# Kernel optimization log

Hardware: AMD Instinct MI355X
Metric: run time of the kernel (lower is better)

Reference implementation:

```python
import jax, jax.numpy as jnp
import numpy as np

N, T, D, P, Q = 256, 4096, 64, 4, 4
COEF_SCALE = 0.15  # keeps ARMA stationary over long T


def setup_inputs() -> dict:
    key = jax.random.key(0)
    k_eps, k_phi, k_theta, k_mu = jax.random.split(key, 4)
    eps = jax.random.normal(k_eps, (N, T, D), dtype=jnp.float32)
    phi = COEF_SCALE * jax.random.normal(k_phi, (D, P), dtype=jnp.float32)
    theta = COEF_SCALE * jax.random.normal(k_theta, (D, Q), dtype=jnp.float32)
    mu = jax.random.normal(k_mu, (D,), dtype=jnp.float32)
    x0 = jnp.zeros((N, D), dtype=jnp.float32)
    return {"eps": eps, "phi": phi, "theta": theta, "mu": mu, "x0": x0}


def reference(eps, phi, theta, mu, x0):
    # eps: (N,T,d); phi: (d,p); theta: (d,q); mu: (d,); x0: (N,d)
    n, t, d = eps.shape
    p = phi.shape[1]
    q = theta.shape[1]
    # x history: most-recent-first, [x0, 0, ..., 0] (matches torch padding of x_hist)
    xh0 = jnp.concatenate([x0[:, :, None], jnp.zeros((n, d, p - 1), eps.dtype)], axis=-1)
    eh0 = jnp.zeros((n, d, q), eps.dtype)  # eps history starts as zeros

    def step(carry, e_t):
        xh, eh = carry  # (n,d,p), (n,d,q)
        ar = jnp.einsum('ndp,dp->nd', xh, phi)
        ma = jnp.einsum('ndq,dq->nd', eh, theta)
        x_t = mu[None, :] + ar + e_t + ma  # (n,d)
        xh = jnp.concatenate([x_t[:, :, None], xh[:, :, :-1]], axis=-1)
        eh = jnp.concatenate([e_t[:, :, None], eh[:, :, :-1]], axis=-1)
        return (xh, eh), x_t

    _, xs = jax.lax.scan(step, (xh0, eh0), jnp.swapaxes(eps, 0, 1))  # xs: (T,N,d)
    return jnp.swapaxes(xs, 0, 1)  # (N,T,d)
```

## Files before the change

kernel.cpp:

```cpp
#include <hip/hip_runtime.h>
#include <stdint.h>


typedef float f32x4 __attribute__((ext_vector_type(4)));

constexpr int N = 256;
constexpr int T = 4096;
constexpr int D = 64;
constexpr int P = 4;
constexpr int Q = 4;

constexpr int K = 8;
constexpr int L = 512;
constexpr int B = 256;
constexpr int U = 16;
constexpr int NB = 4;
constexpr int NDMA = (U * D * sizeof(float)) / 1024;

__global__ __launch_bounds__(64, 2)
void arma_wide_kernel(const float* __restrict__ eps,
                      const float* __restrict__ phi,
                      const float* __restrict__ theta,
                      const float* __restrict__ mu,
                      const float* __restrict__ x0,
                      float* __restrict__ out) {
    const int lane = threadIdx.x;
    const int k = blockIdx.x % K;
    const int n = blockIdx.x / K;

    const float ph0 = phi[lane * P + 0];
    const float ph1 = phi[lane * P + 1];
    const float ph2 = phi[lane * P + 2];
    const float ph3 = phi[lane * P + 3];
    const float th0 = theta[lane * Q + 0];
    const float th1 = theta[lane * Q + 1];
    const float th2 = theta[lane * Q + 2];
    const float th3 = theta[lane * Q + 3];
    const float m   = mu[lane];

    const int t0   = k * L;
    const int ts   = (k == 0) ? 0 : t0 - B;
    const int tend = t0 + L;
    const int nit  = (tend - ts) / U;
    const int SB   = (t0 - ts) / U;

    const float* gbase = eps + (size_t)n * T * D;
    float*       obase = out + (size_t)n * T * D;

    const int lt  = lane >> 4;
    const int ld4 = (lane & 15) * 4;

    __shared__ float lbuf[NB][U * D];
    __shared__ float sbuf[U * D];

    float x1, x2, x3, x4, e1, e2, e3, e4;
    x1 = x2 = x3 = x4 = 0.f;
    e1 = e2 = e3 = e4 = 0.f;
    if (k == 0) {
        x1 = x0[n * D + lane];
    } else {
        e1 = gbase[(size_t)(ts - 1) * D + lane];
        e2 = gbase[(size_t)(ts - 2) * D + lane];
        e3 = gbase[(size_t)(ts - 3) * D + lane];
        e4 = gbase[(size_t)(ts - 4) * D + lane];
    }

    auto issue = [&](int b, int t) {
#pragma unroll
        for (int i = 0; i < NDMA; ++i) {
            const float* src = gbase + (size_t)(t + i * 4 + lt) * D + ld4;
            __builtin_amdgcn_global_load_lds(
                (const __attribute__((address_space(1))) void*)src,
                (__attribute__((address_space(3))) void*)&lbuf[b][i * 256],
                16, 0, 0);
        }
    };

    auto compute = [&](int b) {
#pragma unroll
        for (int u = 0; u < U; ++u) {
            const float e = lbuf[b][u * D + lane];
            float acc = m + e;
            acc = fmaf(th0, e1, acc);
            acc = fmaf(th1, e2, acc);
            acc = fmaf(th2, e3, acc);
            acc = fmaf(th3, e4, acc);
            acc = fmaf(ph3, x4, acc);
            acc = fmaf(ph2, x3, acc);
            acc = fmaf(ph1, x2, acc);
            const float x = fmaf(ph0, x1, acc);
            x4 = x3; x3 = x2; x2 = x1; x1 = x;
            e4 = e3; e3 = e2; e2 = e1; e1 = e;
            sbuf[u * D + lane] = x;
        }
    };

    auto flush = [&](int t) {
#pragma unroll
        for (int i = 0; i < 4; ++i) {
            const int row = i * 4 + lt;
            const f32x4 v = *reinterpret_cast<const f32x4*>(&sbuf[row * D + ld4]);
            __builtin_nontemporal_store(
                v, reinterpret_cast<f32x4*>(&obase[(size_t)(t + row) * D + ld4]));
        }
    };

    issue(0, ts);
    issue(1, ts + U);
    issue(2, ts + 2 * U);

    for (int j = 0; j < nit; ++j) {
        const int t = ts + j * U;
        int tpre = t + 3 * U;
        if (tpre > tend - U) tpre = tend - U;
        issue((j + 3) & (NB - 1), tpre);

        const int d = j - SB;
        if (d <= 0) {
            asm volatile("s_waitcnt vmcnt(12)" ::: "memory");
        } else if (d == 1) {
            asm volatile("s_waitcnt vmcnt(16)" ::: "memory");
        } else if (d == 2) {
            asm volatile("s_waitcnt vmcnt(20)" ::: "memory");
        } else {
            asm volatile("s_waitcnt vmcnt(24)" ::: "memory");
        }
        __builtin_amdgcn_sched_barrier(0);

        compute(j & (NB - 1));
        if (j >= SB) flush(t);
    }
}

extern "C" void kernel_launch(void* const* d_in, const int* in_sizes, int n_in,
                              void* d_out, int out_size, void* d_ws, size_t ws_size,
                              hipStream_t stream) {
    const float* eps   = (const float*)d_in[0];
    const float* phi   = (const float*)d_in[1];
    const float* theta = (const float*)d_in[2];
    const float* mu    = (const float*)d_in[3];
    const float* x0    = (const float*)d_in[4];
    float* out = (float*)d_out;

    arma_wide_kernel<<<dim3(N * K), dim3(64), 0, stream>>>(eps, phi, theta, mu, x0, out);
}
```

Before: 107.7 us.

## Halve time-chunk count and deepen LDS prefetch pipeline to five stages

Splits each series into 4 time chunks of 1024 steps instead of 8 of 512. This cuts the redundant 256-step warm-up reads that every non-first chunk recomputes. Prefetch depth goes from 3 to 5 stages over 8 LDS buffers, with an explicit epilogue loop and retuned vmcnt waits, and the clamped duplicate prefetches at the tail are removed. The trade-off is half as many blocks and longer serial recurrences per block, which may reduce memory-level parallelism across the GPU.

```diff
diff --git a/kernel.cpp b/kernel.cpp
--- a/kernel.cpp
+++ b/kernel.cpp
@@ -10,20 +10,21 @@
 constexpr int P = 4;
 constexpr int Q = 4;
 
-constexpr int K = 8;
-constexpr int L = 512;
+constexpr int K = 4;
+constexpr int L = 1024;
 constexpr int B = 256;
 constexpr int U = 16;
-constexpr int NB = 4;
+constexpr int NB = 8;
+constexpr int DP = 5;
 constexpr int NDMA = (U * D * sizeof(float)) / 1024;
 
-__global__ __launch_bounds__(64, 2)
-void arma_wide_kernel(const float* __restrict__ eps,
-                      const float* __restrict__ phi,
-                      const float* __restrict__ theta,
-                      const float* __restrict__ mu,
-                      const float* __restrict__ x0,
-                      float* __restrict__ out) {
+__global__ __launch_bounds__(64, 1)
+void arma_k4_kernel(const float* __restrict__ eps,
+                    const float* __restrict__ phi,
+                    const float* __restrict__ theta,
+                    const float* __restrict__ mu,
+                    const float* __restrict__ x0,
+                    float* __restrict__ out) {
     const int lane = threadIdx.x;
     const int k = blockIdx.x % K;
     const int n = blockIdx.x / K;
@@ -105,30 +106,51 @@
         }
     };
 
-    issue(0, ts);
-    issue(1, ts + U);
-    issue(2, ts + 2 * U);
+#pragma unroll
+    for (int s = 0; s < DP; ++s) issue(s & (NB - 1), ts + s * U);
 
-    for (int j = 0; j < nit; ++j) {
+    for (int j = 0; j < nit - DP; ++j) {
         const int t = ts + j * U;
-        int tpre = t + 3 * U;
-        if (tpre > tend - U) tpre = tend - U;
-        issue((j + 3) & (NB - 1), tpre);
+        issue((j + DP) & (NB - 1), t + DP * U);
 
         const int d = j - SB;
         if (d <= 0) {
-            asm volatile("s_waitcnt vmcnt(12)" ::: "memory");
+            asm volatile("s_waitcnt vmcnt(20)" ::: "memory");
         } else if (d == 1) {
-            asm volatile("s_waitcnt vmcnt(16)" ::: "memory");
+            asm volatile("s_waitcnt vmcnt(24)" ::: "memory");
         } else if (d == 2) {
-            asm volatile("s_waitcnt vmcnt(20)" ::: "memory");
+            asm volatile("s_waitcnt vmcnt(28)" ::: "memory");
+        } else if (d == 3) {
+            asm volatile("s_waitcnt vmcnt(32)" ::: "memory");
+        } else if (d == 4) {
+            asm volatile("s_waitcnt vmcnt(36)" ::: "memory");
         } else {
-            asm volatile("s_waitcnt vmcnt(24)" ::: "memory");
+            asm volatile("s_waitcnt vmcnt(40)" ::: "memory");
         }
         __builtin_amdgcn_sched_barrier(0);
 
         compute(j & (NB - 1));
         if (j >= SB) flush(t);
+    }
+
+    for (int j = nit - DP; j < nit; ++j) {
+        const int t = ts + j * U;
+        const int e = nit - 1 - j;
+        if (e == 4) {
+            asm volatile("s_waitcnt vmcnt(36)" ::: "memory");
+        } else if (e == 3) {
+            asm volatile("s_waitcnt vmcnt(32)" ::: "memory");
+        } else if (e == 2) {
+            asm volatile("s_waitcnt vmcnt(28)" ::: "memory");
+        } else if (e == 1) {
+            asm volatile("s_waitcnt vmcnt(24)" ::: "memory");
+        } else {
+            asm volatile("s_waitcnt vmcnt(20)" ::: "memory");
+        }
+        __builtin_amdgcn_sched_barrier(0);
+
+        compute(j & (NB - 1));
+        flush(t);
     }
 }
 
@@ -142,5 +164,5 @@
     const float* x0    = (const float*)d_in[4];
     float* out = (float*)d_out;
 
-    arma_wide_kernel<<<dim3(N * K), dim3(64), 0, stream>>>(eps, phi, theta, mu, x0, out);
+    arma_k4_kernel<<<dim3(N * K), dim3(64), 0, stream>>>(eps, phi, theta, mu, x0, out);
 }
```

After: 106.1 us. No clear change (-1.4%).

## Balance time chunks so all blocks run equal step counts

Applied to the files above, without the earlier changes.

Resizes the time-chunk partition so the first chunk (no warmup) is longer and later chunks (with warmup overlap) are shorter, giving every block the same iteration count. Replaces the clamped prefetch loop with a fixed-trip main loop plus a peeled drain with explicit waitcnts, avoiding redundant tail loads. This removes load imbalance where the first chunk's blocks finished early, at the cost of more rigid constant-dependent code.

```diff
diff --git a/kernel.cpp b/kernel.cpp
--- a/kernel.cpp
+++ b/kernel.cpp
@@ -10,20 +10,27 @@
 constexpr int P = 4;
 constexpr int Q = 4;
 
-constexpr int K = 8;
-constexpr int L = 512;
-constexpr int B = 256;
-constexpr int U = 16;
+constexpr int K  = 8;
+constexpr int B  = 256;
+constexpr int L0 = 736;
+constexpr int LK = 480;
+constexpr int U  = 16;
 constexpr int NB = 4;
+constexpr int DP = 3;
+constexpr int NIT = L0 / U;
 constexpr int NDMA = (U * D * sizeof(float)) / 1024;
 
+static_assert(L0 == (T + (K - 1) * B) / K, "balanced chunk arithmetic");
+static_assert(L0 % U == 0 && LK % U == 0 && B % U == 0, "stage alignment");
+static_assert(L0 + (K - 1) * LK == T, "chunks cover T");
+
 __global__ __launch_bounds__(64, 2)
-void arma_wide_kernel(const float* __restrict__ eps,
-                      const float* __restrict__ phi,
-                      const float* __restrict__ theta,
-                      const float* __restrict__ mu,
-                      const float* __restrict__ x0,
-                      float* __restrict__ out) {
+void arma_bal_kernel(const float* __restrict__ eps,
+                     const float* __restrict__ phi,
+                     const float* __restrict__ theta,
+                     const float* __restrict__ mu,
+                     const float* __restrict__ x0,
+                     float* __restrict__ out) {
     const int lane = threadIdx.x;
     const int k = blockIdx.x % K;
     const int n = blockIdx.x / K;
@@ -38,11 +45,9 @@
     const float th3 = theta[lane * Q + 3];
     const float m   = mu[lane];
 
-    const int t0   = k * L;
-    const int ts   = (k == 0) ? 0 : t0 - B;
-    const int tend = t0 + L;
-    const int nit  = (tend - ts) / U;
-    const int SB   = (t0 - ts) / U;
+    const int t0 = (k == 0) ? 0 : L0 + (k - 1) * LK;
+    const int ts = (k == 0) ? 0 : t0 - B;
+    const int SB = (k == 0) ? 0 : B / U;
 
     const float* gbase = eps + (size_t)n * T * D;
     float*       obase = out + (size_t)n * T * D;
@@ -105,15 +110,12 @@
         }
     };
 
-    issue(0, ts);
-    issue(1, ts + U);
-    issue(2, ts + 2 * U);
+#pragma unroll
+    for (int s = 0; s < DP; ++s) issue(s, ts + s * U);
 
-    for (int j = 0; j < nit; ++j) {
+    for (int j = 0; j < NIT - DP; ++j) {
         const int t = ts + j * U;
-        int tpre = t + 3 * U;
-        if (tpre > tend - U) tpre = tend - U;
-        issue((j + 3) & (NB - 1), tpre);
+        issue((j + DP) & (NB - 1), t + DP * U);
 
         const int d = j - SB;
         if (d <= 0) {
@@ -130,6 +132,22 @@
         compute(j & (NB - 1));
         if (j >= SB) flush(t);
     }
+
+    for (int j = NIT - DP; j < NIT; ++j) {
+        const int t = ts + j * U;
+        const int e = NIT - 1 - j;
+        if (e == 2) {
+            asm volatile("s_waitcnt vmcnt(20)" ::: "memory");
+        } else if (e == 1) {
+            asm volatile("s_waitcnt vmcnt(16)" ::: "memory");
+        } else {
+            asm volatile("s_waitcnt vmcnt(12)" ::: "memory");
+        }
+        __builtin_amdgcn_sched_barrier(0);
+
+        compute(j & (NB - 1));
+        flush(t);
+    }
 }
 
 extern "C" void kernel_launch(void* const* d_in, const int* in_sizes, int n_in,
@@ -142,5 +160,5 @@
     const float* x0    = (const float*)d_in[4];
     float* out = (float*)d_out;
 
-    arma_wide_kernel<<<dim3(N * K), dim3(64), 0, stream>>>(eps, phi, theta, mu, x0, out);
+    arma_bal_kernel<<<dim3(N * K), dim3(64), 0, stream>>>(eps, phi, theta, mu, x0, out);
 }
```

Result: faster. 105.3 us (-2.2%).
